# Optimization experiments

Hardware: AMD Instinct MI355X
Metric: run time of the kernel (lower is better)

The kernel has to match this reference:

```python
import jax, jax.numpy as jnp
import numpy as np

L, B, S, D = 8, 1, 4096, 2048
H, KVH, HD = 16, 2, 128
Q = 32
THETA = 1e6
MROPE = (16, 24, 24)  # mrope_section, sums to HD//2
EPS = 1e-6


def setup_inputs() -> dict:
    key = jax.random.key(0)
    ks = jax.random.split(key, 8)
    hidden_states = jax.random.normal(ks[0], (L, B, S, D), dtype=jnp.float32)
    ln_w = jax.random.uniform(ks[1], (L, D), dtype=jnp.float32, minval=0.5, maxval=1.5)
    q_w = jax.random.normal(ks[2], (L, D, H * HD), dtype=jnp.float32) * 0.02
    q_b = jax.random.normal(ks[3], (L, H * HD), dtype=jnp.float32) * 0.02
    k_w = jax.random.normal(ks[4], (L, D, KVH * HD), dtype=jnp.float32) * 0.02
    k_b = jax.random.normal(ks[5], (L, KVH * HD), dtype=jnp.float32) * 0.02
    position_ids = jax.random.randint(ks[6], (3, B, S), 0, S, dtype=jnp.int32)
    q_idx = jnp.sort(jax.random.randint(ks[7], (Q,), 0, S, dtype=jnp.int32))
    return {"hidden_states": hidden_states, "ln_w": ln_w, "q_w": q_w, "q_b": q_b,
            "k_w": k_w, "k_b": k_b, "position_ids": position_ids, "q_idx": q_idx}


def _rot_half(x):
    h = x.shape[-1] // 2
    return jnp.concatenate([-x[..., h:], x[..., :h]], axis=-1)


def _mrope_combine(t):
    # t: (3, B, S, HD). Split last dim per 2*mrope_section, chunk i taken from axis i%3.
    parts, off = [], 0
    for i, sec in enumerate(MROPE):
        w = 2 * sec
        parts.append(t[i % 3, :, :, off:off + w])
        off += w
    return jnp.concatenate(parts, axis=-1)[:, None, :, :]  # (B, 1, S, HD)


def reference(hidden_states, ln_w, q_w, q_b, k_w, k_b, position_ids, q_idx):
    # Rotary embeddings from 3D mRoPE position ids
    inv_freq = 1.0 / (THETA ** (jnp.arange(0, HD, 2, dtype=jnp.float32) / HD))  # (HD/2,)
    freqs = position_ids.astype(jnp.float32)[..., None] * inv_freq  # (3, B, S, HD/2)
    emb = jnp.concatenate([freqs, freqs], axis=-1)  # (3, B, S, HD)
    cos = _mrope_combine(jnp.cos(emb))  # (B, 1, S, HD)
    sin = _mrope_combine(jnp.sin(emb))
    cos_q = cos[:, :, q_idx, :]  # (B, 1, Q, HD)
    sin_q = sin[:, :, q_idx, :]
    # Eager causal mask sliced at query rows: (Q, S)
    mask_add = jnp.where(jnp.arange(S)[None, :] > q_idx[:, None], -1e9, 0.0).astype(jnp.float32)

    scale = 1.0 / np.sqrt(HD).astype(np.float32)

    def per_layer(hs, lw, qw, qb, kw, kb):
        # RMSNorm (input_layernorm)
        var = jnp.mean(jnp.square(hs), axis=-1, keepdims=True)
        x = hs * jax.lax.rsqrt(var + EPS) * lw  # (B, S, D)
        xq = x[:, q_idx, :]  # (B, Q, D)
        k = (jnp.einsum('bsd,de->bse', x, kw) + kb).reshape(B, S, KVH, HD).transpose(0, 2, 1, 3)
        q = (jnp.einsum('bqd,de->bqe', xq, qw) + qb).reshape(B, Q, H, HD).transpose(0, 2, 1, 3)
        k = jnp.repeat(k, H // KVH, axis=1)  # repeat_kv -> (B, H, S, HD)
        k = k * cos + _rot_half(k) * sin
        q = q * cos_q + _rot_half(q) * sin_q
        scores = jnp.einsum('bhqd,bhkd->bhqk', q, k) * scale  # (B, H, Q, S)
        scores = scores + mask_add[None, None]
        return jax.nn.softmax(scores.astype(jnp.float32), axis=-1)

    return jax.vmap(per_layer)(hidden_states, ln_w, q_w, q_b, k_w, k_b)  # (L, B, H, Q, S)
```

## Files before the change

kernel.cpp:

```cpp
#include <hip/hip_runtime.h>
#include <hip/hip_bf16.h>
#include <math.h>

#define LYR 8
#define SEQ 4096
#define DIM 2048
#define NH 16
#define HD 128
#define NQ 32
#define NKV 256
#define NQE 2048

typedef __attribute__((ext_vector_type(8))) short short8;
typedef __attribute__((ext_vector_type(4))) float f32x4;

#define WS_IRQ   0
#define WS_ABLOB 256
#define WS_COS   524544
#define WS_SIN   1048832
#define WS_QBUF  1573120
#define WS_PART  2097408
#define WS_W2    4194560
#define WS_KBLOB 8388864
#define WS_QBLOB 16777472

__device__ __forceinline__ short f2bf(float x) {
  __hip_bfloat16 h = __float2bfloat16(x);
  return *(short*)&h;
}
__device__ __forceinline__ float bf2f(short s) {
  unsigned u = ((unsigned)(unsigned short)s) << 16;
  return __uint_as_float(u);
}

#define GLOAD16(srcp, dstp) \
  __builtin_amdgcn_global_load_lds( \
      (const __attribute__((address_space(1))) unsigned int*)(srcp), \
      (__attribute__((address_space(3))) unsigned int*)(dstp), 16, 0, 0)

#define RBAR() asm volatile("s_waitcnt lgkmcnt(0)\n\ts_barrier" ::: "memory")

__global__ __launch_bounds__(256) void prep_kernel(
    const float* __restrict__ ln_w, const float* __restrict__ k_w,
    short* __restrict__ W2) {
  int kb = blockIdx.x, l = blockIdx.y, t = threadIdx.x;
  const float* kwl = k_w + (size_t)l * DIM * NKV;
  const float* lnl = ln_w + l * DIM;
  short* blob = W2 + (size_t)(l * 64 + kb) * 16384;
  #pragma unroll
  for (int i = 0; i < 4; ++i) {
    int p = t + i * 256;
    int fi = p >> 6, lane = p & 63;
    int n = fi * 16 + (lane & 15);
    int k0 = kb * 32 + (lane >> 4) * 8;
    short hi8[8], lo8[8];
    #pragma unroll
    for (int e = 0; e < 8; ++e) {
      float v = lnl[k0 + e] * kwl[(size_t)(k0 + e) * NKV + n];
      short h = f2bf(v);
      hi8[e] = h;
      lo8[e] = f2bf(v - bf2f(h));
    }
    *(short8*)(blob + p * 8) = *(short8*)hi8;
    *(short8*)(blob + 8192 + p * 8) = *(short8*)lo8;
  }
}

__global__ __launch_bounds__(256) void rmsq_kernel(const float* __restrict__ hs,
                                                   const int* __restrict__ q_idx,
                                                   float* __restrict__ irq) {
  int qi = blockIdx.x, l = blockIdx.y, t = threadIdx.x;
  int s = q_idx[qi];
  const float* row = hs + ((size_t)l * SEQ + s) * DIM;
  float4 v0 = *(const float4*)(row + t * 4);
  float4 v1 = *(const float4*)(row + t * 4 + 1024);
  float acc = v0.x*v0.x + v0.y*v0.y + v0.z*v0.z + v0.w*v0.w
            + v1.x*v1.x + v1.y*v1.y + v1.z*v1.z + v1.w*v1.w;
  #pragma unroll
  for (int off = 32; off >= 1; off >>= 1) acc += __shfl_down(acc, off);
  __shared__ float red[4];
  if ((t & 63) == 0) red[t >> 6] = acc;
  __syncthreads();
  if (t == 0) {
    float tot = red[0] + red[1] + red[2] + red[3];
    irq[l * NQ + qi] = rsqrtf(tot / (float)DIM + 1e-6f);
  }
}

__global__ void cossin_kernel(const int* __restrict__ pos_ids,
                              float* __restrict__ cost, float* __restrict__ sint) {
  int idx = blockIdx.x * 256 + threadIdx.x;
  int s = idx >> 7, d = idx & 127;
  int t = (d < 32) ? 0 : (d < 80 ? 1 : 2);
  int j = d & 63;
  double invf = pow(1000000.0, -(double)j / 64.0);
  double ph = (double)pos_ids[t * SEQ + s] * invf;
  cost[idx] = (float)cos(ph);
  sint[idx] = (float)sin(ph);
}

__global__ __launch_bounds__(256) void xqt_kernel(
    const float* __restrict__ hs, const float* __restrict__ ln_w,
    const int* __restrict__ q_idx, const float* __restrict__ irq,
    short* __restrict__ Ablob) {
  __shared__ int qix[32];
  __shared__ float qir[32];
  int l = blockIdx.x, t = threadIdx.x;
  if (t < 32) { qix[t] = q_idx[t]; qir[t] = irq[l * NQ + t]; }
  __syncthreads();
  int lane = t & 63, g4 = t >> 6;
  short* base = Ablob + (size_t)l * 131072;
  int row = lane & 15, kgl = lane >> 4;
  for (int i = 0; i < 64; ++i) {
    int group = g4 * 64 + i;
    int kb = group >> 2, half = (group >> 1) & 1, mf = group & 1;
    int r = row + mf * 16;
    int k0 = kb * 32 + kgl * 8;
    const float* src = hs + ((size_t)l * SEQ + qix[r]) * DIM + k0;
    const float* lnp = ln_w + l * DIM + k0;
    float ir = qir[r];
    float4 v0 = *(const float4*)src;
    float4 v1 = *(const float4*)(src + 4);
    float4 w0 = *(const float4*)lnp;
    float4 w1 = *(const float4*)(lnp + 4);
    float av[8] = {v0.x*w0.x, v0.y*w0.y, v0.z*w0.z, v0.w*w0.w,
                   v1.x*w1.x, v1.y*w1.y, v1.z*w1.z, v1.w*w1.w};
    short o8[8];
    #pragma unroll
    for (int e = 0; e < 8; ++e) {
      float v = av[e] * ir;
      short h = f2bf(v);
      o8[e] = half ? f2bf(v - bf2f(h)) : h;
    }
    *(short8*)(base + group * 512 + lane * 8) = *(short8*)o8;
  }
}

__global__ __launch_bounds__(256) void kgemm_kernel(
    const float* __restrict__ hs, const short* __restrict__ W2,
    const float* __restrict__ k_b, const float* __restrict__ cost,
    const float* __restrict__ sint, short* __restrict__ Kblob) {
  __shared__ __align__(1024) char SM[67072];

  int t = threadIdx.x;
  int fid = blockIdx.x;
  int l = fid & 7, sb = fid >> 3;
  int s0 = sb * 64;
  int lane = t & 63, w = t >> 6;
  int fr = lane & 15, kg = lane >> 4;
  int arow = t >> 2, akg = t & 3;

  const float* hrow = hs + ((size_t)l * SEQ + s0 + arow) * DIM + akg * 8;
  const char* wbase = (const char*)(W2 + (size_t)l * 64 * 16384);
  const char* wfrag = wbase + w * 1024 + lane * 16;

  int amf = arow >> 4;
  int awoff = amf * 1024 + (((akg * 16 + (arow & 15)) * 16) ^ (akg << 5));
  int aroff = (lane * 16) ^ ((lane >> 4) << 5);

  f32x4 acc[4][4];
  #pragma unroll
  for (int mf = 0; mf < 4; ++mf)
    #pragma unroll
    for (int nf = 0; nf < 4; ++nf) acc[mf][nf] = (f32x4){0.f, 0.f, 0.f, 0.f};
  float sq = 0.f;
  float4 rA0, rA1, rB0, rB1;
  short8 B0h[4], B0l[4], B1h[4], B1l[4];

  {
    #pragma unroll
    for (int nf = 0; nf < 4; ++nf) {
      B0h[nf] = *(const short8*)(wfrag + nf * 4096);
      B0l[nf] = *(const short8*)(wfrag + nf * 4096 + 16384);
    }
    float4 a0 = *(const float4*)(hrow);
    float4 a1 = *(const float4*)(hrow + 4);
    float av[8] = {a0.x, a0.y, a0.z, a0.w, a1.x, a1.y, a1.z, a1.w};
    short hi8[8], lo8[8];
    #pragma unroll
    for (int e = 0; e < 8; ++e) {
      sq += av[e] * av[e];
      short h = f2bf(av[e]);
      hi8[e] = h;
      lo8[e] = f2bf(av[e] - bf2f(h));
    }
    *(short8*)(SM + awoff) = *(short8*)hi8;
    *(short8*)(SM + 4096 + awoff) = *(short8*)lo8;
    rA0 = *(const float4*)(hrow + 32);
    rA1 = *(const float4*)(hrow + 36);
  }
  RBAR();

#define KSTEP(KB, CA0, CA1, NA0, NA1, UBH, UBL, PBH, PBL) do { \
    int buf_ = (KB) & 1; \
    char* asb_ = SM + buf_ * 8192; \
    if ((KB) < 63) { \
      const char* bsrc_ = wfrag + (size_t)((KB) + 1) * 32768; \
      _Pragma("unroll") \
      for (int nf = 0; nf < 4; ++nf) { \
        PBH[nf] = *(const short8*)(bsrc_ + nf * 4096); \
        PBL[nf] = *(const short8*)(bsrc_ + nf * 4096 + 16384); \
      } \
    } \
    if ((KB) < 62) { \
      NA0 = *(const float4*)(hrow + ((KB) + 2) * 32); \
      NA1 = *(const float4*)(hrow + ((KB) + 2) * 32 + 4); \
    } \
    short8 ah_[4], al_[4]; \
    _Pragma("unroll") \
    for (int mf = 0; mf < 4; ++mf) { \
      ah_[mf] = *(const short8*)(asb_ + mf * 1024 + aroff); \
      al_[mf] = *(const short8*)(asb_ + 4096 + mf * 1024 + aroff); \
    } \
    __builtin_amdgcn_s_setprio(1); \
    _Pragma("unroll") \
    for (int nf = 0; nf < 4; ++nf) { \
      _Pragma("unroll") \
      for (int mf = 0; mf < 4; ++mf) { \
        acc[mf][nf] = __builtin_amdgcn_mfma_f32_16x16x32_bf16(ah_[mf], UBH[nf], acc[mf][nf], 0, 0, 0); \
        acc[mf][nf] = __builtin_amdgcn_mfma_f32_16x16x32_bf16(ah_[mf], UBL[nf], acc[mf][nf], 0, 0, 0); \
        acc[mf][nf] = __builtin_amdgcn_mfma_f32_16x16x32_bf16(al_[mf], UBH[nf], acc[mf][nf], 0, 0, 0); \
      } \
    } \
    __builtin_amdgcn_s_setprio(0); \
    if ((KB) < 63) { \
      char* asn_ = SM + (buf_ ^ 1) * 8192; \
      float av_[8] = {CA0.x, CA0.y, CA0.z, CA0.w, CA1.x, CA1.y, CA1.z, CA1.w}; \
      short hi8_[8], lo8_[8]; \
      _Pragma("unroll") \
      for (int e = 0; e < 8; ++e) { \
        sq += av_[e] * av_[e]; \
        short h_ = f2bf(av_[e]); \
        hi8_[e] = h_; \
        lo8_[e] = f2bf(av_[e] - bf2f(h_)); \
      } \
      *(short8*)(asn_ + awoff) = *(short8*)hi8_; \
      *(short8*)(asn_ + 4096 + awoff) = *(short8*)lo8_; \
    } \
    RBAR(); \
  } while (0)

  for (int kb2 = 0; kb2 < 32; ++kb2) {
    KSTEP(2 * kb2,     rA0, rA1, rB0, rB1, B0h, B0l, B1h, B1l);
    KSTEP(2 * kb2 + 1, rB0, rB1, rA0, rA1, B1h, B1l, B0h, B0l);
  }
#undef KSTEP

  sq += __shfl_xor(sq, 1);
  sq += __shfl_xor(sq, 2);
  float* irs = (float*)(SM + 66560);
  if ((t & 3) == 0) irs[arow] = rsqrtf(sq / (float)DIM + 1e-6f);
  __syncthreads();

  float* Kraw = (float*)SM;
  int j = w * 16 + fr;
  float bias0 = k_b[l * NKV + j];
  float bias1 = k_b[l * NKV + j + 64];
  float bias2 = k_b[l * NKV + j + 128];
  float bias3 = k_b[l * NKV + j + 192];
  #pragma unroll
  for (int mf = 0; mf < 4; ++mf) {
    #pragma unroll
    for (int r = 0; r < 4; ++r) {
      int row = mf * 16 + kg * 4 + r;
      int s = s0 + row;
      float ir = irs[row];
      float v0 = acc[mf][0][r] * ir + bias0;
      float v1 = acc[mf][1][r] * ir + bias1;
      float v2 = acc[mf][2][r] * ir + bias2;
      float v3 = acc[mf][3][r] * ir + bias3;
      float cj = cost[s * HD + j], sj = sint[s * HD + j];
      float cj2 = cost[s * HD + j + 64], sj2 = sint[s * HD + j + 64];
      float* kr = Kraw + row * 260;
      kr[j]       = v0 * cj - v1 * sj;
      kr[j + 64]  = v1 * cj2 + v0 * sj2;
      kr[j + 128] = v2 * cj - v3 * sj;
      kr[j + 192] = v3 * cj2 + v2 * sj2;
    }
  }
  __syncthreads();

  int kc = sb >> 1, fb = (sb & 1) * 4;
  #pragma unroll
  for (int i = 0; i < 8; ++i) {
    int c = t + i * 256;
    int lc = c & 63, fl = (c >> 6) & 3, ts = (c >> 8) & 3, kv = c >> 10;
    int key = fl * 16 + (lc & 15);
    int d0 = kv * 128 + ts * 32 + (lc >> 4) * 8;
    float4 x0 = *(const float4*)(Kraw + key * 260 + d0);
    float4 x1 = *(const float4*)(Kraw + key * 260 + d0 + 4);
    float av[8] = {x0.x, x0.y, x0.z, x0.w, x1.x, x1.y, x1.z, x1.w};
    short hi8[8], lo8[8];
    #pragma unroll
    for (int e = 0; e < 8; ++e) {
      short h = f2bf(av[e]);
      hi8[e] = h;
      lo8[e] = f2bf(av[e] - bf2f(h));
    }
    short* bb = Kblob + (size_t)((l * 2 + kv) * 32 + kc) * 32768
              + (size_t)((ts * 2 + 0) * 8 + fb + fl) * 512 + lc * 8;
    *(short8*)bb = *(short8*)hi8;
    *(short8*)(bb + 4096) = *(short8*)lo8;
  }
}

__global__ __launch_bounds__(512) void qgemm_kernel(
    const float* __restrict__ q_w, const short* __restrict__ Ablob,
    float* __restrict__ part) {
  __shared__ __align__(1024) char SM[131072];
  int t = threadIdx.x;
  int nc = blockIdx.x, ks = blockIdx.y, l = blockIdx.z;
  int lane = t & 63, w = t >> 6;
  int fr = lane & 15, kg = lane >> 4;
  const char* abase = (const char*)(Ablob + (size_t)l * 131072 + (size_t)ks * 32768);
  const float* qwl = q_w + (size_t)l * DIM * NQE;

  #pragma unroll
  for (int c = 0; c < 8; ++c) {
    int chunk = w * 8 + c;
    GLOAD16(abase + chunk * 1024 + lane * 16, SM + chunk * 1024);
  }
  #pragma unroll
  for (int c = 0; c < 4; ++c) {
    int r = w * 4 + c;
    GLOAD16((const char*)(qwl + (size_t)(ks * 512 + r) * NQE + nc * 256) + lane * 16,
            SM + 65536 + r * 1024 + lane * 16);
  }
  f32x4 acc[2][2];
  #pragma unroll
  for (int mf = 0; mf < 2; ++mf)
    #pragma unroll
    for (int nf = 0; nf < 2; ++nf) acc[mf][nf] = (f32x4){0.f, 0.f, 0.f, 0.f};
  __syncthreads();

  for (int ts = 0; ts < 16; ++ts) {
    int buf = ts & 1;
    if (ts < 15) {
      #pragma unroll
      for (int c = 0; c < 4; ++c) {
        int r = w * 4 + c;
        GLOAD16((const char*)(qwl + (size_t)(ks * 512 + (ts + 1) * 32 + r) * NQE + nc * 256) + lane * 16,
                SM + 65536 + (buf ^ 1) * 32768 + r * 1024 + lane * 16);
      }
    }
    short8 ah[2], al[2];
    #pragma unroll
    for (int mf = 0; mf < 2; ++mf) {
      ah[mf] = *(const short8*)(SM + ts * 4096 + mf * 1024 + lane * 16);
      al[mf] = *(const short8*)(SM + ts * 4096 + 2048 + mf * 1024 + lane * 16);
    }
    const float* bt = (const float*)(SM + 65536 + buf * 32768);
    #pragma unroll
    for (int nf = 0; nf < 2; ++nf) {
      int c = w * 32 + nf * 16 + fr;
      short bh8[8], bl8[8];
      #pragma unroll
      for (int e = 0; e < 8; ++e) {
        float v = bt[(kg * 8 + e) * 256 + c];
        short h = f2bf(v);
        bh8[e] = h;
        bl8[e] = f2bf(v - bf2f(h));
      }
      short8 bh = *(short8*)bh8, bl = *(short8*)bl8;
      #pragma unroll
      for (int mf = 0; mf < 2; ++mf) {
        acc[mf][nf] = __builtin_amdgcn_mfma_f32_16x16x32_bf16(ah[mf], bh, acc[mf][nf], 0, 0, 0);
        acc[mf][nf] = __builtin_amdgcn_mfma_f32_16x16x32_bf16(ah[mf], bl, acc[mf][nf], 0, 0, 0);
        acc[mf][nf] = __builtin_amdgcn_mfma_f32_16x16x32_bf16(al[mf], bh, acc[mf][nf], 0, 0, 0);
      }
    }
    __syncthreads();
  }

  #pragma unroll
  for (int mf = 0; mf < 2; ++mf) {
    #pragma unroll
    for (int r = 0; r < 4; ++r) {
      int row = mf * 16 + kg * 4 + r;
      float* prow = part + ((size_t)((ks * LYR + l) * NQ + row)) * NQE + nc * 256;
      #pragma unroll
      for (int nf = 0; nf < 2; ++nf) {
        int col = w * 32 + nf * 16 + fr;
        prow[col] = acc[mf][nf][r];
      }
    }
  }
}

__global__ __launch_bounds__(256) void qred_kernel(
    const float* __restrict__ part, const float* __restrict__ q_b,
    float* __restrict__ Qbuf) {
  int idx = blockIdx.x * 256 + threadIdx.x;
  int n = idx & 2047, q = (idx >> 11) & 31, l = idx >> 16;
  float v = q_b[l * NQE + n];
  #pragma unroll
  for (int ks = 0; ks < 4; ++ks)
    v += part[((size_t)((ks * LYR + l) * NQ + q)) * NQE + n];
  Qbuf[((size_t)l * NQ + q) * NQE + n] = v;
}

__global__ __launch_bounds__(256) void qpack_kernel(
    const float* __restrict__ Qbuf, const float* __restrict__ cost,
    const float* __restrict__ sint, const int* __restrict__ q_idx,
    short* __restrict__ Qblob) {
  int kv = blockIdx.x, l = blockIdx.y, t = threadIdx.x;
  short* blob = Qblob + (size_t)(l * 2 + kv) * 65536;
  #pragma unroll
  for (int i = 0; i < 16; ++i) {
    int p = t + i * 256;
    int ts = p >> 10, f = (p >> 6) & 15, lane = p & 63;
    int row = f * 16 + (lane & 15);
    int hh = row >> 5, q = row & 31;
    int h = kv * 8 + hh;
    int d0 = ts * 32 + (lane >> 4) * 8;
    int s = q_idx[q];
    const float* qrow = Qbuf + ((size_t)l * NQ + q) * NQE + h * HD;
    const float* ct = cost + s * HD;
    const float* st = sint + s * HD;
    short hi8[8], lo8[8];
    #pragma unroll
    for (int e = 0; e < 8; ++e) {
      int d = d0 + e;
      float x = qrow[d];
      float xp = qrow[d ^ 64];
      float v = (d < 64) ? (x * ct[d] - xp * st[d]) : (x * ct[d] + xp * st[d]);
      short h2 = f2bf(v);
      hi8[e] = h2;
      lo8[e] = f2bf(v - bf2f(h2));
    }
    *(short8*)(blob + ((ts * 2 + 0) * 16 + f) * 512 + lane * 8) = *(short8*)hi8;
    *(short8*)(blob + ((ts * 2 + 1) * 16 + f) * 512 + lane * 8) = *(short8*)lo8;
  }
}

__global__ __launch_bounds__(512) void scores_kernel(
    const short* __restrict__ Qblob, const short* __restrict__ Kblob,
    const int* __restrict__ q_idx, float* __restrict__ out) {
  __shared__ short Qs[2][16384];
  __shared__ short Ks[2][8192];
  __shared__ int qiv[32];
  int t = threadIdx.x;
  int kc = blockIdx.x, kv = blockIdx.y, l = blockIdx.z;
  int lane = t & 63, w = t >> 6;
  int wm = w >> 1, wn = w & 1;
  if (t < 32) qiv[t] = q_idx[t];
  const char* qsrc = (const char*)(Qblob + (size_t)(l * 2 + kv) * 65536);
  const char* ksrc = (const char*)(Kblob + (size_t)((l * 2 + kv) * 32 + kc) * 32768);
  #pragma unroll
  for (int c = 0; c < 4; ++c) {
    int off = (w * 4 + c) * 1024;
    GLOAD16(qsrc + off + lane * 16, (char*)Qs[0] + off);
  }
  #pragma unroll
  for (int c = 0; c < 2; ++c) {
    int off = (w * 2 + c) * 1024;
    GLOAD16(ksrc + off + lane * 16, (char*)Ks[0] + off);
  }
  f32x4 acc[4][4];
  #pragma unroll
  for (int mf = 0; mf < 4; ++mf)
    #pragma unroll
    for (int nf = 0; nf < 4; ++nf) acc[mf][nf] = (f32x4){0.f, 0.f, 0.f, 0.f};
  __syncthreads();
  for (int ts = 0; ts < 4; ++ts) {
    int buf = ts & 1;
    if (ts < 3) {
      const char* qs = qsrc + (ts + 1) * 32768;
      const char* ks = ksrc + (ts + 1) * 16384;
      #pragma unroll
      for (int c = 0; c < 4; ++c) {
        int off = (w * 4 + c) * 1024;
        GLOAD16(qs + off + lane * 16, (char*)Qs[(ts + 1) & 1] + off);
      }
      #pragma unroll
      for (int c = 0; c < 2; ++c) {
        int off = (w * 2 + c) * 1024;
        GLOAD16(ks + off + lane * 16, (char*)Ks[(ts + 1) & 1] + off);
      }
    }
    short8 ah[4], al[4];
    #pragma unroll
    for (int mf = 0; mf < 4; ++mf) {
      int f = wm * 4 + mf;
      ah[mf] = *(const short8*)(Qs[buf] + f * 512 + lane * 8);
      al[mf] = *(const short8*)(Qs[buf] + 8192 + f * 512 + lane * 8);
    }
    #pragma unroll
    for (int nf = 0; nf < 4; ++nf) {
      int f = wn * 4 + nf;
      short8 bh = *(const short8*)(Ks[buf] + f * 512 + lane * 8);
      short8 bl = *(const short8*)(Ks[buf] + 4096 + f * 512 + lane * 8);
      #pragma unroll
      for (int mf = 0; mf < 4; ++mf) {
        acc[mf][nf] = __builtin_amdgcn_mfma_f32_16x16x32_bf16(ah[mf], bh, acc[mf][nf], 0, 0, 0);
        acc[mf][nf] = __builtin_amdgcn_mfma_f32_16x16x32_bf16(ah[mf], bl, acc[mf][nf], 0, 0, 0);
        acc[mf][nf] = __builtin_amdgcn_mfma_f32_16x16x32_bf16(al[mf], bh, acc[mf][nf], 0, 0, 0);
      }
    }
    __syncthreads();
  }
  const float scale = 0.088388347648318447f;
  #pragma unroll
  for (int mf = 0; mf < 4; ++mf) {
    #pragma unroll
    for (int r = 0; r < 4; ++r) {
      int rr = wm * 64 + mf * 16 + (lane >> 4) * 4 + r;
      int hh = rr >> 5, q = rr & 31;
      int qv = qiv[q];
      float* orow = out + (((size_t)(l * NH + kv * 8 + hh)) * NQ + q) * SEQ;
      #pragma unroll
      for (int nf = 0; nf < 4; ++nf) {
        int key = kc * 128 + (wn * 4 + nf) * 16 + (lane & 15);
        orow[key] = (key > qv) ? -1e9f : acc[mf][nf][r] * scale;
      }
    }
  }
}

__global__ __launch_bounds__(256) void softmax_kernel(float* __restrict__ out) {
  size_t row = blockIdx.x;
  float* p = out + row * SEQ;
  int t = threadIdx.x;
  float4 v[4];
  float mx = -1e30f;
  #pragma unroll
  for (int i = 0; i < 4; ++i) {
    v[i] = *(const float4*)(p + t * 4 + i * 1024);
    mx = fmaxf(mx, fmaxf(fmaxf(v[i].x, v[i].y), fmaxf(v[i].z, v[i].w)));
  }
  #pragma unroll
  for (int off = 32; off >= 1; off >>= 1) mx = fmaxf(mx, __shfl_xor(mx, off));
  __shared__ float red[4];
  if ((t & 63) == 0) red[t >> 6] = mx;
  __syncthreads();
  mx = fmaxf(fmaxf(red[0], red[1]), fmaxf(red[2], red[3]));
  __syncthreads();
  float sum = 0.f;
  #pragma unroll
  for (int i = 0; i < 4; ++i) {
    v[i].x = __expf(v[i].x - mx); v[i].y = __expf(v[i].y - mx);
    v[i].z = __expf(v[i].z - mx); v[i].w = __expf(v[i].w - mx);
    sum += v[i].x + v[i].y + v[i].z + v[i].w;
  }
  #pragma unroll
  for (int off = 32; off >= 1; off >>= 1) sum += __shfl_xor(sum, off);
  if ((t & 63) == 0) red[t >> 6] = sum;
  __syncthreads();
  sum = red[0] + red[1] + red[2] + red[3];
  float inv = 1.f / sum;
  #pragma unroll
  for (int i = 0; i < 4; ++i) {
    v[i].x *= inv; v[i].y *= inv; v[i].z *= inv; v[i].w *= inv;
    *(float4*)(p + t * 4 + i * 1024) = v[i];
  }
}

extern "C" void kernel_launch(void* const* d_in, const int* in_sizes, int n_in,
                              void* d_out, int out_size, void* d_ws, size_t ws_size,
                              hipStream_t stream) {
  const float* hs   = (const float*)d_in[0];
  const float* ln_w = (const float*)d_in[1];
  const float* q_w  = (const float*)d_in[2];
  const float* q_b  = (const float*)d_in[3];
  const float* k_w  = (const float*)d_in[4];
  const float* k_b  = (const float*)d_in[5];
  const int* pos    = (const int*)d_in[6];
  const int* qidx   = (const int*)d_in[7];
  float* out = (float*)d_out;
  float* ws = (float*)d_ws;
  float* irq   = ws + WS_IRQ;
  short* Ablob = (short*)(ws + WS_ABLOB);
  float* cost  = ws + WS_COS;
  float* sint  = ws + WS_SIN;
  float* Qbuf  = ws + WS_QBUF;
  float* part  = ws + WS_PART;
  short* W2    = (short*)(ws + WS_W2);
  short* Kblob = (short*)(ws + WS_KBLOB);
  short* Qblob = (short*)(ws + WS_QBLOB);

  prep_kernel<<<dim3(64, LYR), 256, 0, stream>>>(ln_w, k_w, W2);
  rmsq_kernel<<<dim3(NQ, LYR), 256, 0, stream>>>(hs, qidx, irq);
  cossin_kernel<<<(SEQ * HD) / 256, 256, 0, stream>>>(pos, cost, sint);
  xqt_kernel<<<LYR, 256, 0, stream>>>(hs, ln_w, qidx, irq, Ablob);
  kgemm_kernel<<<512, 256, 0, stream>>>(hs, W2, k_b, cost, sint, Kblob);
  qgemm_kernel<<<dim3(8, 4, LYR), 512, 0, stream>>>(q_w, Ablob, part);
  qred_kernel<<<2048, 256, 0, stream>>>(part, q_b, Qbuf);
  qpack_kernel<<<dim3(2, LYR), 256, 0, stream>>>(Qbuf, cost, sint, qidx, Qblob);
  scores_kernel<<<dim3(32, 2, LYR), 512, 0, stream>>>(Qblob, Kblob, qidx, out);
  softmax_kernel<<<LYR * NH * NQ, 256, 0, stream>>>(out);
}
```

Baseline: 279.8 us.

## Split K-projection GEMM reduction across two wave groups per block

The K GEMM kernel now runs 512 threads per block. Two groups of four waves each handle half of the 2048-wide reduction dimension, and their partial accumulators and sum-of-squares are combined through shared memory before the RMS scale, bias and rotary epilogue. The A-register double prefetch and the MFMA priority hints are dropped, and launch bounds now request higher occupancy. This halves the serial K-loop length per wave to add latency hiding, at the cost of an extra LDS reduction pass and more shared memory per block.

```diff
diff --git a/kernel.cpp b/kernel.cpp
--- a/kernel.cpp
+++ b/kernel.cpp
@@ -136,27 +136,30 @@
   }
 }
 
-__global__ __launch_bounds__(256) void kgemm_kernel(
+__global__ __launch_bounds__(512, 4) void kgemm_kernel(
     const float* __restrict__ hs, const short* __restrict__ W2,
     const float* __restrict__ k_b, const float* __restrict__ cost,
     const float* __restrict__ sint, short* __restrict__ Kblob) {
-  __shared__ __align__(1024) char SM[67072];
+  __shared__ __align__(1024) char SM[67584];
 
   int t = threadIdx.x;
   int fid = blockIdx.x;
   int l = fid & 7, sb = fid >> 3;
   int s0 = sb * 64;
   int lane = t & 63, w = t >> 6;
+  int wn = w & 3, g = w >> 2;
   int fr = lane & 15, kg = lane >> 4;
-  int arow = t >> 2, akg = t & 3;
-
-  const float* hrow = hs + ((size_t)l * SEQ + s0 + arow) * DIM + akg * 8;
+  int tg = t & 255;
+  int arow = tg >> 2, akg = tg & 3;
+
+  const float* hrow = hs + ((size_t)l * SEQ + s0 + arow) * DIM + g * 1024 + akg * 8;
   const char* wbase = (const char*)(W2 + (size_t)l * 64 * 16384);
-  const char* wfrag = wbase + w * 1024 + lane * 16;
-
+  const char* wfrag = wbase + (size_t)g * 1048576 + wn * 1024 + lane * 16;
+
+  int abase = g * 16384;
   int amf = arow >> 4;
-  int awoff = amf * 1024 + (((akg * 16 + (arow & 15)) * 16) ^ (akg << 5));
-  int aroff = (lane * 16) ^ ((lane >> 4) << 5);
+  int awoff = abase + amf * 1024 + (((akg * 16 + (arow & 15)) * 16) ^ (akg << 5));
+  int aroff = abase + ((lane * 16) ^ ((lane >> 4) << 5));
 
   f32x4 acc[4][4];
   #pragma unroll
@@ -164,7 +167,6 @@
     #pragma unroll
     for (int nf = 0; nf < 4; ++nf) acc[mf][nf] = (f32x4){0.f, 0.f, 0.f, 0.f};
   float sq = 0.f;
-  float4 rA0, rA1, rB0, rB1;
   short8 B0h[4], B0l[4], B1h[4], B1l[4];
 
   {
@@ -186,15 +188,16 @@
     }
     *(short8*)(SM + awoff) = *(short8*)hi8;
     *(short8*)(SM + 4096 + awoff) = *(short8*)lo8;
-    rA0 = *(const float4*)(hrow + 32);
-    rA1 = *(const float4*)(hrow + 36);
   }
   RBAR();
 
-#define KSTEP(KB, CA0, CA1, NA0, NA1, UBH, UBL, PBH, PBL) do { \
+#define KSTEP(KB, UBH, UBL, PBH, PBL) do { \
     int buf_ = (KB) & 1; \
-    char* asb_ = SM + buf_ * 8192; \
-    if ((KB) < 63) { \
+    const char* asb_ = SM + buf_ * 8192; \
+    float4 a0_, a1_; \
+    if ((KB) < 31) { \
+      a0_ = *(const float4*)(hrow + ((KB) + 1) * 32); \
+      a1_ = *(const float4*)(hrow + ((KB) + 1) * 32 + 4); \
       const char* bsrc_ = wfrag + (size_t)((KB) + 1) * 32768; \
       _Pragma("unroll") \
       for (int nf = 0; nf < 4; ++nf) { \
@@ -202,17 +205,12 @@
         PBL[nf] = *(const short8*)(bsrc_ + nf * 4096 + 16384); \
       } \
     } \
-    if ((KB) < 62) { \
-      NA0 = *(const float4*)(hrow + ((KB) + 2) * 32); \
-      NA1 = *(const float4*)(hrow + ((KB) + 2) * 32 + 4); \
-    } \
     short8 ah_[4], al_[4]; \
     _Pragma("unroll") \
     for (int mf = 0; mf < 4; ++mf) { \
       ah_[mf] = *(const short8*)(asb_ + mf * 1024 + aroff); \
       al_[mf] = *(const short8*)(asb_ + 4096 + mf * 1024 + aroff); \
     } \
-    __builtin_amdgcn_s_setprio(1); \
     _Pragma("unroll") \
     for (int nf = 0; nf < 4; ++nf) { \
       _Pragma("unroll") \
@@ -222,10 +220,9 @@
         acc[mf][nf] = __builtin_amdgcn_mfma_f32_16x16x32_bf16(al_[mf], UBH[nf], acc[mf][nf], 0, 0, 0); \
       } \
     } \
-    __builtin_amdgcn_s_setprio(0); \
-    if ((KB) < 63) { \
+    if ((KB) < 31) { \
       char* asn_ = SM + (buf_ ^ 1) * 8192; \
-      float av_[8] = {CA0.x, CA0.y, CA0.z, CA0.w, CA1.x, CA1.y, CA1.z, CA1.w}; \
+      float av_[8] = {a0_.x, a0_.y, a0_.z, a0_.w, a1_.x, a1_.y, a1_.z, a1_.w}; \
       short hi8_[8], lo8_[8]; \
       _Pragma("unroll") \
       for (int e = 0; e < 8; ++e) { \
@@ -240,55 +237,78 @@
     RBAR(); \
   } while (0)
 
-  for (int kb2 = 0; kb2 < 32; ++kb2) {
-    KSTEP(2 * kb2,     rA0, rA1, rB0, rB1, B0h, B0l, B1h, B1l);
-    KSTEP(2 * kb2 + 1, rB0, rB1, rA0, rA1, B1h, B1l, B0h, B0l);
+  for (int kb2 = 0; kb2 < 16; ++kb2) {
+    KSTEP(2 * kb2,     B0h, B0l, B1h, B1l);
+    KSTEP(2 * kb2 + 1, B1h, B1l, B0h, B0l);
   }
 #undef KSTEP
 
   sq += __shfl_xor(sq, 1);
   sq += __shfl_xor(sq, 2);
-  float* irs = (float*)(SM + 66560);
-  if ((t & 3) == 0) irs[arow] = rsqrtf(sq / (float)DIM + 1e-6f);
-  __syncthreads();
-
-  float* Kraw = (float*)SM;
-  int j = w * 16 + fr;
-  float bias0 = k_b[l * NKV + j];
-  float bias1 = k_b[l * NKV + j + 64];
-  float bias2 = k_b[l * NKV + j + 128];
-  float bias3 = k_b[l * NKV + j + 192];
-  #pragma unroll
-  for (int mf = 0; mf < 4; ++mf) {
-    #pragma unroll
-    for (int r = 0; r < 4; ++r) {
-      int row = mf * 16 + kg * 4 + r;
-      int s = s0 + row;
-      float ir = irs[row];
-      float v0 = acc[mf][0][r] * ir + bias0;
-      float v1 = acc[mf][1][r] * ir + bias1;
-      float v2 = acc[mf][2][r] * ir + bias2;
-      float v3 = acc[mf][3][r] * ir + bias3;
-      float cj = cost[s * HD + j], sj = sint[s * HD + j];
-      float cj2 = cost[s * HD + j + 64], sj2 = sint[s * HD + j + 64];
-      float* kr = Kraw + row * 260;
-      kr[j]       = v0 * cj - v1 * sj;
-      kr[j + 64]  = v1 * cj2 + v0 * sj2;
-      kr[j + 128] = v2 * cj - v3 * sj;
-      kr[j + 192] = v3 * cj2 + v2 * sj2;
+  float* sqpart = (float*)(SM + 66560);
+  if ((t & 3) == 0) sqpart[g * 64 + arow] = sq;
+
+  float* X = (float*)SM;
+  int j = wn * 16 + fr;
+  if (g == 1) {
+    #pragma unroll
+    for (int mf = 0; mf < 4; ++mf) {
+      #pragma unroll
+      for (int r = 0; r < 4; ++r) {
+        int row = mf * 16 + kg * 4 + r;
+        #pragma unroll
+        for (int nf = 0; nf < 4; ++nf)
+          X[row * 260 + j + nf * 64] = acc[mf][nf][r];
+      }
+    }
+  }
+  __syncthreads();
+
+  float* irs = (float*)(SM + 67072);
+  if (t < 64)
+    irs[t] = rsqrtf((sqpart[t] + sqpart[64 + t]) / (float)DIM + 1e-6f);
+  __syncthreads();
+
+  if (g == 0) {
+    float bias0 = k_b[l * NKV + j];
+    float bias1 = k_b[l * NKV + j + 64];
+    float bias2 = k_b[l * NKV + j + 128];
+    float bias3 = k_b[l * NKV + j + 192];
+    #pragma unroll
+    for (int mf = 0; mf < 4; ++mf) {
+      #pragma unroll
+      for (int r = 0; r < 4; ++r) {
+        int row = mf * 16 + kg * 4 + r;
+        int s = s0 + row;
+        float ir = irs[row];
+        float p0 = X[row * 260 + j]       + acc[mf][0][r];
+        float p1 = X[row * 260 + j + 64]  + acc[mf][1][r];
+        float p2 = X[row * 260 + j + 128] + acc[mf][2][r];
+        float p3 = X[row * 260 + j + 192] + acc[mf][3][r];
+        float v0 = p0 * ir + bias0;
+        float v1 = p1 * ir + bias1;
+        float v2 = p2 * ir + bias2;
+        float v3 = p3 * ir + bias3;
+        float cj = cost[s * HD + j], sj = sint[s * HD + j];
+        float cj2 = cost[s * HD + j + 64], sj2 = sint[s * HD + j + 64];
+        X[row * 260 + j]       = v0 * cj - v1 * sj;
+        X[row * 260 + j + 64]  = v1 * cj2 + v0 * sj2;
+        X[row * 260 + j + 128] = v2 * cj - v3 * sj;
+        X[row * 260 + j + 192] = v3 * cj2 + v2 * sj2;
+      }
     }
   }
   __syncthreads();
 
   int kc = sb >> 1, fb = (sb & 1) * 4;
   #pragma unroll
-  for (int i = 0; i < 8; ++i) {
-    int c = t + i * 256;
+  for (int i = 0; i < 4; ++i) {
+    int c = t + i * 512;
     int lc = c & 63, fl = (c >> 6) & 3, ts = (c >> 8) & 3, kv = c >> 10;
     int key = fl * 16 + (lc & 15);
     int d0 = kv * 128 + ts * 32 + (lc >> 4) * 8;
-    float4 x0 = *(const float4*)(Kraw + key * 260 + d0);
-    float4 x1 = *(const float4*)(Kraw + key * 260 + d0 + 4);
+    float4 x0 = *(const float4*)(X + key * 260 + d0);
+    float4 x1 = *(const float4*)(X + key * 260 + d0 + 4);
     float av[8] = {x0.x, x0.y, x0.z, x0.w, x1.x, x1.y, x1.z, x1.w};
     short hi8[8], lo8[8];
     #pragma unroll
@@ -582,7 +602,7 @@
   rmsq_kernel<<<dim3(NQ, LYR), 256, 0, stream>>>(hs, qidx, irq);
   cossin_kernel<<<(SEQ * HD) / 256, 256, 0, stream>>>(pos, cost, sint);
   xqt_kernel<<<LYR, 256, 0, stream>>>(hs, ln_w, qidx, irq, Ablob);
-  kgemm_kernel<<<512, 256, 0, stream>>>(hs, W2, k_b, cost, sint, Kblob);
+  kgemm_kernel<<<512, 512, 0, stream>>>(hs, W2, k_b, cost, sint, Kblob);
   qgemm_kernel<<<dim3(8, 4, LYR), 512, 0, stream>>>(q_w, Ablob, part);
   qred_kernel<<<2048, 256, 0, stream>>>(part, q_b, Qbuf);
   qpack_kernel<<<dim3(2, LYR), 256, 0, stream>>>(Qbuf, cost, sint, qidx, Qblob);
```

After: 454.5 us. +62.5%, slower.

## Batch four K-steps per LDS stage to cut barriers in K-projection GEMM

Applied to the files above, without the earlier changes.

The K-projection GEMM main loop now stages four 32-wide K slices per LDS buffer (32 KB each, double-buffered) instead of one slice per buffer. This cuts workgroup barriers from one per K-step to one per four K-steps, and prefetches activations two register sets deep. The s_setprio hints around the MFMA block are dropped. In exchange it uses slightly more shared memory and more live registers, which may reduce occupancy.

```diff
diff --git a/kernel.cpp b/kernel.cpp
--- a/kernel.cpp
+++ b/kernel.cpp
@@ -140,7 +140,7 @@
     const float* __restrict__ hs, const short* __restrict__ W2,
     const float* __restrict__ k_b, const float* __restrict__ cost,
     const float* __restrict__ sint, short* __restrict__ Kblob) {
-  __shared__ __align__(1024) char SM[67072];
+  __shared__ __align__(1024) char SM[67584];
 
   int t = threadIdx.x;
   int fid = blockIdx.x;
@@ -154,8 +154,7 @@
   const char* wbase = (const char*)(W2 + (size_t)l * 64 * 16384);
   const char* wfrag = wbase + w * 1024 + lane * 16;
 
-  int amf = arow >> 4;
-  int awoff = amf * 1024 + (((akg * 16 + (arow & 15)) * 16) ^ (akg << 5));
+  int awoff = (arow >> 4) * 1024 + (((akg * 16 + (arow & 15)) * 16) ^ (akg << 5));
   int aroff = (lane * 16) ^ ((lane >> 4) << 5);
 
   f32x4 acc[4][4];
@@ -164,17 +163,13 @@
     #pragma unroll
     for (int nf = 0; nf < 4; ++nf) acc[mf][nf] = (f32x4){0.f, 0.f, 0.f, 0.f};
   float sq = 0.f;
-  float4 rA0, rA1, rB0, rB1;
   short8 B0h[4], B0l[4], B1h[4], B1l[4];
-
-  {
-    #pragma unroll
-    for (int nf = 0; nf < 4; ++nf) {
-      B0h[nf] = *(const short8*)(wfrag + nf * 4096);
-      B0l[nf] = *(const short8*)(wfrag + nf * 4096 + 16384);
-    }
-    float4 a0 = *(const float4*)(hrow);
-    float4 a1 = *(const float4*)(hrow + 4);
+  float4 LA0, LA1, LB0, LB1;
+
+  #pragma unroll
+  for (int s = 0; s < 4; ++s) {
+    float4 a0 = *(const float4*)(hrow + s * 32);
+    float4 a1 = *(const float4*)(hrow + s * 32 + 4);
     float av[8] = {a0.x, a0.y, a0.z, a0.w, a1.x, a1.y, a1.z, a1.w};
     short hi8[8], lo8[8];
     #pragma unroll
@@ -184,35 +179,38 @@
       hi8[e] = h;
       lo8[e] = f2bf(av[e] - bf2f(h));
     }
-    *(short8*)(SM + awoff) = *(short8*)hi8;
-    *(short8*)(SM + 4096 + awoff) = *(short8*)lo8;
-    rA0 = *(const float4*)(hrow + 32);
-    rA1 = *(const float4*)(hrow + 36);
-  }
+    *(short8*)(SM + s * 8192 + awoff) = *(short8*)hi8;
+    *(short8*)(SM + s * 8192 + 4096 + awoff) = *(short8*)lo8;
+  }
+  #pragma unroll
+  for (int nf = 0; nf < 4; ++nf) {
+    B0h[nf] = *(const short8*)(wfrag + nf * 4096);
+    B0l[nf] = *(const short8*)(wfrag + nf * 4096 + 16384);
+  }
+  LA0 = *(const float4*)(hrow + 128); LA1 = *(const float4*)(hrow + 132);
+  LB0 = *(const float4*)(hrow + 160); LB1 = *(const float4*)(hrow + 164);
   RBAR();
 
-#define KSTEP(KB, CA0, CA1, NA0, NA1, UBH, UBL, PBH, PBL) do { \
-    int buf_ = (KB) & 1; \
-    char* asb_ = SM + buf_ * 8192; \
-    if ((KB) < 63) { \
-      const char* bsrc_ = wfrag + (size_t)((KB) + 1) * 32768; \
+#define GSTEP(S, RD, WR, HA, BF, UBH, UBL, PBH, PBL, L0, L1, DOLD, DOW, DOPB) do { \
+    if (DOPB) { \
+      const char* bsrc_ = (BF) + (size_t)((S) + 1) * 32768; \
       _Pragma("unroll") \
       for (int nf = 0; nf < 4; ++nf) { \
         PBH[nf] = *(const short8*)(bsrc_ + nf * 4096); \
         PBL[nf] = *(const short8*)(bsrc_ + nf * 4096 + 16384); \
       } \
     } \
-    if ((KB) < 62) { \
-      NA0 = *(const float4*)(hrow + ((KB) + 2) * 32); \
-      NA1 = *(const float4*)(hrow + ((KB) + 2) * 32 + 4); \
+    float4 na0_, na1_; \
+    if (DOLD) { \
+      na0_ = *(const float4*)((HA) + ((S) + 6) * 32); \
+      na1_ = *(const float4*)((HA) + ((S) + 6) * 32 + 4); \
     } \
     short8 ah_[4], al_[4]; \
     _Pragma("unroll") \
     for (int mf = 0; mf < 4; ++mf) { \
-      ah_[mf] = *(const short8*)(asb_ + mf * 1024 + aroff); \
-      al_[mf] = *(const short8*)(asb_ + 4096 + mf * 1024 + aroff); \
+      ah_[mf] = *(const short8*)((RD) + (S) * 8192 + mf * 1024 + aroff); \
+      al_[mf] = *(const short8*)((RD) + (S) * 8192 + 4096 + mf * 1024 + aroff); \
     } \
-    __builtin_amdgcn_s_setprio(1); \
     _Pragma("unroll") \
     for (int nf = 0; nf < 4; ++nf) { \
       _Pragma("unroll") \
@@ -222,10 +220,8 @@
         acc[mf][nf] = __builtin_amdgcn_mfma_f32_16x16x32_bf16(al_[mf], UBH[nf], acc[mf][nf], 0, 0, 0); \
       } \
     } \
-    __builtin_amdgcn_s_setprio(0); \
-    if ((KB) < 63) { \
-      char* asn_ = SM + (buf_ ^ 1) * 8192; \
-      float av_[8] = {CA0.x, CA0.y, CA0.z, CA0.w, CA1.x, CA1.y, CA1.z, CA1.w}; \
+    if (DOW) { \
+      float av_[8] = {L0.x, L0.y, L0.z, L0.w, L1.x, L1.y, L1.z, L1.w}; \
       short hi8_[8], lo8_[8]; \
       _Pragma("unroll") \
       for (int e = 0; e < 8; ++e) { \
@@ -234,17 +230,45 @@
         hi8_[e] = h_; \
         lo8_[e] = f2bf(av_[e] - bf2f(h_)); \
       } \
-      *(short8*)(asn_ + awoff) = *(short8*)hi8_; \
-      *(short8*)(asn_ + 4096 + awoff) = *(short8*)lo8_; \
+      *(short8*)((WR) + (S) * 8192 + awoff) = *(short8*)hi8_; \
+      *(short8*)((WR) + (S) * 8192 + 4096 + awoff) = *(short8*)lo8_; \
     } \
-    RBAR(); \
+    if (DOLD) { L0 = na0_; L1 = na1_; } \
   } while (0)
 
-  for (int kb2 = 0; kb2 < 32; ++kb2) {
-    KSTEP(2 * kb2,     rA0, rA1, rB0, rB1, B0h, B0l, B1h, B1l);
-    KSTEP(2 * kb2 + 1, rB0, rB1, rA0, rA1, B1h, B1l, B0h, B0l);
-  }
-#undef KSTEP
+  for (int kb2 = 0; kb2 < 7; ++kb2) {
+    const float* hA = hrow + kb2 * 256;
+    const char* bfA = wfrag + (size_t)kb2 * 262144;
+    GSTEP(0, SM, SM + 32768, hA, bfA, B0h, B0l, B1h, B1l, LA0, LA1, 1, 1, 1);
+    GSTEP(1, SM, SM + 32768, hA, bfA, B1h, B1l, B0h, B0l, LB0, LB1, 1, 1, 1);
+    GSTEP(2, SM, SM + 32768, hA, bfA, B0h, B0l, B1h, B1l, LA0, LA1, 1, 1, 1);
+    GSTEP(3, SM, SM + 32768, hA, bfA, B1h, B1l, B0h, B0l, LB0, LB1, 1, 1, 1);
+    RBAR();
+    const float* hB = hA + 128;
+    const char* bfB = bfA + 131072;
+    GSTEP(0, SM + 32768, SM, hB, bfB, B0h, B0l, B1h, B1l, LA0, LA1, 1, 1, 1);
+    GSTEP(1, SM + 32768, SM, hB, bfB, B1h, B1l, B0h, B0l, LB0, LB1, 1, 1, 1);
+    GSTEP(2, SM + 32768, SM, hB, bfB, B0h, B0l, B1h, B1l, LA0, LA1, 1, 1, 1);
+    GSTEP(3, SM + 32768, SM, hB, bfB, B1h, B1l, B0h, B0l, LB0, LB1, 1, 1, 1);
+    RBAR();
+  }
+  {
+    const float* hA = hrow + 1792;
+    const char* bf = wfrag + (size_t)14 * 131072;
+    GSTEP(0, SM, SM + 32768, hA, bf, B0h, B0l, B1h, B1l, LA0, LA1, 1, 1, 1);
+    GSTEP(1, SM, SM + 32768, hA, bf, B1h, B1l, B0h, B0l, LB0, LB1, 1, 1, 1);
+    GSTEP(2, SM, SM + 32768, hA, bf, B0h, B0l, B1h, B1l, LA0, LA1, 0, 1, 1);
+    GSTEP(3, SM, SM + 32768, hA, bf, B1h, B1l, B0h, B0l, LB0, LB1, 0, 1, 1);
+    RBAR();
+  }
+  {
+    const char* bf = wfrag + (size_t)15 * 131072;
+    GSTEP(0, SM + 32768, SM, hrow, bf, B0h, B0l, B1h, B1l, LA0, LA1, 0, 0, 1);
+    GSTEP(1, SM + 32768, SM, hrow, bf, B1h, B1l, B0h, B0l, LB0, LB1, 0, 0, 1);
+    GSTEP(2, SM + 32768, SM, hrow, bf, B0h, B0l, B1h, B1l, LA0, LA1, 0, 0, 1);
+    GSTEP(3, SM + 32768, SM, hrow, bf, B1h, B1l, B0h, B0l, LB0, LB1, 0, 0, 0);
+  }
+#undef GSTEP
 
   sq += __shfl_xor(sq, 1);
   sq += __shfl_xor(sq, 2);
```

Measured after the change: 301.1 us. 7.6% more time.

## Split K-projection GEMM across KV heads to double block count and occupancy

Applied to the files above, without the earlier changes.

The K GEMM kernel now gives each block one KV head (128 output columns) instead of both, which doubles the grid to 1024 blocks and halves the accumulators and shared memory per block. Launch bounds request 4 blocks per CU. The A-tile prefetch depth drops from two steps to one and the MFMA priority hints are removed. In exchange, each hidden-state tile is now loaded, squared and converted to split bf16 twice (once per head), and the shallower prefetch exposes more global-load latency per step.

```diff
diff --git a/kernel.cpp b/kernel.cpp
--- a/kernel.cpp
+++ b/kernel.cpp
@@ -136,15 +136,15 @@
   }
 }
 
-__global__ __launch_bounds__(256) void kgemm_kernel(
+__global__ __launch_bounds__(256, 4) void kgemm_kernel(
     const float* __restrict__ hs, const short* __restrict__ W2,
     const float* __restrict__ k_b, const float* __restrict__ cost,
     const float* __restrict__ sint, short* __restrict__ Kblob) {
-  __shared__ __align__(1024) char SM[67072];
+  __shared__ __align__(1024) char SM[34816];
 
   int t = threadIdx.x;
   int fid = blockIdx.x;
-  int l = fid & 7, sb = fid >> 3;
+  int l = fid & 7, nh = (fid >> 3) & 1, sb = fid >> 4;
   int s0 = sb * 64;
   int lane = t & 63, w = t >> 6;
   int fr = lane & 15, kg = lane >> 4;
@@ -152,27 +152,24 @@
 
   const float* hrow = hs + ((size_t)l * SEQ + s0 + arow) * DIM + akg * 8;
   const char* wbase = (const char*)(W2 + (size_t)l * 64 * 16384);
-  const char* wfrag = wbase + w * 1024 + lane * 16;
-
-  int amf = arow >> 4;
-  int awoff = amf * 1024 + (((akg * 16 + (arow & 15)) * 16) ^ (akg << 5));
+  const char* wfrag = wbase + (nh * 8 + w) * 1024 + lane * 16;
+
+  int awoff = (arow >> 4) * 1024 + (((akg * 16 + (arow & 15)) * 16) ^ (akg << 5));
   int aroff = (lane * 16) ^ ((lane >> 4) << 5);
 
-  f32x4 acc[4][4];
+  f32x4 acc[4][2];
   #pragma unroll
   for (int mf = 0; mf < 4; ++mf)
     #pragma unroll
-    for (int nf = 0; nf < 4; ++nf) acc[mf][nf] = (f32x4){0.f, 0.f, 0.f, 0.f};
+    for (int nf = 0; nf < 2; ++nf) acc[mf][nf] = (f32x4){0.f, 0.f, 0.f, 0.f};
   float sq = 0.f;
-  float4 rA0, rA1, rB0, rB1;
-  short8 B0h[4], B0l[4], B1h[4], B1l[4];
+  short8 B0h[2], B0l[2], B1h[2], B1l[2];
 
   {
-    #pragma unroll
-    for (int nf = 0; nf < 4; ++nf) {
-      B0h[nf] = *(const short8*)(wfrag + nf * 4096);
-      B0l[nf] = *(const short8*)(wfrag + nf * 4096 + 16384);
-    }
+    B0h[0] = *(const short8*)(wfrag);
+    B0l[0] = *(const short8*)(wfrag + 16384);
+    B0h[1] = *(const short8*)(wfrag + 4096);
+    B0l[1] = *(const short8*)(wfrag + 4096 + 16384);
     float4 a0 = *(const float4*)(hrow);
     float4 a1 = *(const float4*)(hrow + 4);
     float av[8] = {a0.x, a0.y, a0.z, a0.w, a1.x, a1.y, a1.z, a1.w};
@@ -186,25 +183,21 @@
     }
     *(short8*)(SM + awoff) = *(short8*)hi8;
     *(short8*)(SM + 4096 + awoff) = *(short8*)lo8;
-    rA0 = *(const float4*)(hrow + 32);
-    rA1 = *(const float4*)(hrow + 36);
   }
   RBAR();
 
-#define KSTEP(KB, CA0, CA1, NA0, NA1, UBH, UBL, PBH, PBL) do { \
+#define KSTEP(KB, UBH, UBL, PBH, PBL) do { \
     int buf_ = (KB) & 1; \
-    char* asb_ = SM + buf_ * 8192; \
+    const char* asb_ = SM + buf_ * 8192; \
+    float4 a0_, a1_; \
     if ((KB) < 63) { \
       const char* bsrc_ = wfrag + (size_t)((KB) + 1) * 32768; \
-      _Pragma("unroll") \
-      for (int nf = 0; nf < 4; ++nf) { \
-        PBH[nf] = *(const short8*)(bsrc_ + nf * 4096); \
-        PBL[nf] = *(const short8*)(bsrc_ + nf * 4096 + 16384); \
-      } \
-    } \
-    if ((KB) < 62) { \
-      NA0 = *(const float4*)(hrow + ((KB) + 2) * 32); \
-      NA1 = *(const float4*)(hrow + ((KB) + 2) * 32 + 4); \
+      PBH[0] = *(const short8*)(bsrc_); \
+      PBL[0] = *(const short8*)(bsrc_ + 16384); \
+      PBH[1] = *(const short8*)(bsrc_ + 4096); \
+      PBL[1] = *(const short8*)(bsrc_ + 4096 + 16384); \
+      a0_ = *(const float4*)(hrow + ((KB) + 1) * 32); \
+      a1_ = *(const float4*)(hrow + ((KB) + 1) * 32 + 4); \
     } \
     short8 ah_[4], al_[4]; \
     _Pragma("unroll") \
@@ -212,9 +205,8 @@
       ah_[mf] = *(const short8*)(asb_ + mf * 1024 + aroff); \
       al_[mf] = *(const short8*)(asb_ + 4096 + mf * 1024 + aroff); \
     } \
-    __builtin_amdgcn_s_setprio(1); \
     _Pragma("unroll") \
-    for (int nf = 0; nf < 4; ++nf) { \
+    for (int nf = 0; nf < 2; ++nf) { \
       _Pragma("unroll") \
       for (int mf = 0; mf < 4; ++mf) { \
         acc[mf][nf] = __builtin_amdgcn_mfma_f32_16x16x32_bf16(ah_[mf], UBH[nf], acc[mf][nf], 0, 0, 0); \
@@ -222,10 +214,9 @@
         acc[mf][nf] = __builtin_amdgcn_mfma_f32_16x16x32_bf16(al_[mf], UBH[nf], acc[mf][nf], 0, 0, 0); \
       } \
     } \
-    __builtin_amdgcn_s_setprio(0); \
     if ((KB) < 63) { \
       char* asn_ = SM + (buf_ ^ 1) * 8192; \
-      float av_[8] = {CA0.x, CA0.y, CA0.z, CA0.w, CA1.x, CA1.y, CA1.z, CA1.w}; \
+      float av_[8] = {a0_.x, a0_.y, a0_.z, a0_.w, a1_.x, a1_.y, a1_.z, a1_.w}; \
       short hi8_[8], lo8_[8]; \
       _Pragma("unroll") \
       for (int e = 0; e < 8; ++e) { \
@@ -241,23 +232,21 @@
   } while (0)
 
   for (int kb2 = 0; kb2 < 32; ++kb2) {
-    KSTEP(2 * kb2,     rA0, rA1, rB0, rB1, B0h, B0l, B1h, B1l);
-    KSTEP(2 * kb2 + 1, rB0, rB1, rA0, rA1, B1h, B1l, B0h, B0l);
+    KSTEP(2 * kb2,     B0h, B0l, B1h, B1l);
+    KSTEP(2 * kb2 + 1, B1h, B1l, B0h, B0l);
   }
 #undef KSTEP
 
   sq += __shfl_xor(sq, 1);
   sq += __shfl_xor(sq, 2);
-  float* irs = (float*)(SM + 66560);
+  float* irs = (float*)(SM + 33792);
   if ((t & 3) == 0) irs[arow] = rsqrtf(sq / (float)DIM + 1e-6f);
   __syncthreads();
 
   float* Kraw = (float*)SM;
   int j = w * 16 + fr;
-  float bias0 = k_b[l * NKV + j];
-  float bias1 = k_b[l * NKV + j + 64];
-  float bias2 = k_b[l * NKV + j + 128];
-  float bias3 = k_b[l * NKV + j + 192];
+  float bias0 = k_b[l * NKV + nh * 128 + j];
+  float bias1 = k_b[l * NKV + nh * 128 + j + 64];
   #pragma unroll
   for (int mf = 0; mf < 4; ++mf) {
     #pragma unroll
@@ -267,28 +256,25 @@
       float ir = irs[row];
       float v0 = acc[mf][0][r] * ir + bias0;
       float v1 = acc[mf][1][r] * ir + bias1;
-      float v2 = acc[mf][2][r] * ir + bias2;
-      float v3 = acc[mf][3][r] * ir + bias3;
       float cj = cost[s * HD + j], sj = sint[s * HD + j];
       float cj2 = cost[s * HD + j + 64], sj2 = sint[s * HD + j + 64];
-      float* kr = Kraw + row * 260;
-      kr[j]       = v0 * cj - v1 * sj;
-      kr[j + 64]  = v1 * cj2 + v0 * sj2;
-      kr[j + 128] = v2 * cj - v3 * sj;
-      kr[j + 192] = v3 * cj2 + v2 * sj2;
-    }
-  }
-  __syncthreads();
-
+      float* kr = Kraw + row * 132;
+      kr[j]      = v0 * cj - v1 * sj;
+      kr[j + 64] = v1 * cj2 + v0 * sj2;
+    }
+  }
+  __syncthreads();
+
+  int kv = nh;
   int kc = sb >> 1, fb = (sb & 1) * 4;
   #pragma unroll
   for (int i = 0; i < 8; ++i) {
     int c = t + i * 256;
-    int lc = c & 63, fl = (c >> 6) & 3, ts = (c >> 8) & 3, kv = c >> 10;
+    int lc = c & 63, fl = (c >> 6) & 3, ts = (c >> 8) & 3;
     int key = fl * 16 + (lc & 15);
-    int d0 = kv * 128 + ts * 32 + (lc >> 4) * 8;
-    float4 x0 = *(const float4*)(Kraw + key * 260 + d0);
-    float4 x1 = *(const float4*)(Kraw + key * 260 + d0 + 4);
+    int d0 = ts * 32 + (lc >> 4) * 8;
+    float4 x0 = *(const float4*)(Kraw + key * 132 + d0);
+    float4 x1 = *(const float4*)(Kraw + key * 132 + d0 + 4);
     float av[8] = {x0.x, x0.y, x0.z, x0.w, x1.x, x1.y, x1.z, x1.w};
     short hi8[8], lo8[8];
     #pragma unroll
@@ -582,7 +568,7 @@
   rmsq_kernel<<<dim3(NQ, LYR), 256, 0, stream>>>(hs, qidx, irq);
   cossin_kernel<<<(SEQ * HD) / 256, 256, 0, stream>>>(pos, cost, sint);
   xqt_kernel<<<LYR, 256, 0, stream>>>(hs, ln_w, qidx, irq, Ablob);
-  kgemm_kernel<<<512, 256, 0, stream>>>(hs, W2, k_b, cost, sint, Kblob);
+  kgemm_kernel<<<1024, 256, 0, stream>>>(hs, W2, k_b, cost, sint, Kblob);
   qgemm_kernel<<<dim3(8, 4, LYR), 512, 0, stream>>>(q_w, Ablob, part);
   qred_kernel<<<2048, 256, 0, stream>>>(part, q_b, Qbuf);
   qpack_kernel<<<dim3(2, LYR), 256, 0, stream>>>(Qbuf, cost, sint, qidx, Qblob);
```

Result: slower. 286.2 us (+2.3%).
